# Optimization experiments

Hardware: AMD Instinct MI355X
Metric: run time of the kernel (lower is better)

The kernel has to match this reference:

```python
import jax, jax.numpy as jnp
import numpy as np

IN_CAPS = 1152
OUT_CAPS = 10
IN_DIM = 8
OUT_DIM = 16
ROUTING_ITERS = 3
BATCH = 512


def squash(s, axis=-1, eps=1e-8):
    # v = (||s||^2 / (1 + ||s||^2)) * s / ||s||
    mag_sq = jnp.sum(s * s, axis=axis, keepdims=True)
    mag = jnp.sqrt(mag_sq + eps)
    return (mag_sq / (1.0 + mag_sq)) * (s / mag)


def setup_inputs() -> dict:
    key = jax.random.key(0)
    kx, kw = jax.random.split(key)
    x = jax.random.normal(kx, (BATCH, IN_CAPS, IN_DIM), dtype=jnp.float32)
    stdv = 1.0 / np.sqrt(IN_CAPS)
    W = jax.random.uniform(kw, (IN_CAPS, OUT_CAPS, OUT_DIM, IN_DIM),
                           minval=-stdv, maxval=stdv, dtype=jnp.float32)
    return {"x": x, "W": W}


def reference(x, W):
    # u_hat[b,i,j,:] = W[i,j] @ x[b,i]  -> [B, 1152, 10, 16]
    u_hat = jnp.einsum('ijde,bie->bijd', W, x)
    u_det = jax.lax.stop_gradient(u_hat)
    b = jnp.zeros((x.shape[0], IN_CAPS, OUT_CAPS), dtype=x.dtype)
    v = None
    for it in range(ROUTING_ITERS):
        c = jax.nn.softmax(b, axis=2)  # softmax over out capsules
        u = u_hat if it == ROUTING_ITERS - 1 else u_det
        s = jnp.einsum('bij,bijd->bjd', c, u)  # [B, 10, 16]
        v = squash(s, axis=-1)
        if it != ROUTING_ITERS - 1:
            # agreement: u_hat . v  -> [B, 1152, 10]
            b = b + jnp.einsum('bijd,bjd->bij', u_det, v)
    return v  # [B, 10, 16]
```

## Files before the change

### kernel.cpp

```cpp
#include <hip/hip_runtime.h>
#include <math.h>

#define J 10
#define BT 16
#define NBT 32
#define NIC 16
#define ICB 72
#define IPW 18
#define JD 160
#define BATCH 512
#define IN_CAPS 1152
#define RTH 256

typedef __attribute__((ext_vector_type(8))) short short8;
typedef __attribute__((ext_vector_type(4))) float f32x4;
typedef __attribute__((ext_vector_type(4))) unsigned uint4v;

__device__ inline short f2bf(float f) {
    union { float f; unsigned u; } v; v.f = f;
    return (short)((v.u + 0x7FFFu + ((v.u >> 16) & 1u)) >> 16);
}
__device__ inline short8 cvt8(float4 a, float4 b) {
    short8 o;
    o[0] = f2bf(a.x); o[1] = f2bf(a.y); o[2] = f2bf(a.z); o[3] = f2bf(a.w);
    o[4] = f2bf(b.x); o[5] = f2bf(b.y); o[6] = f2bf(b.z); o[7] = f2bf(b.w);
    return o;
}
__device__ inline float bf2f(short s) {
    union { unsigned u; float f; } v; v.u = ((unsigned)(unsigned short)s) << 16;
    return v.f;
}

__global__ __launch_bounds__(256) void convert_w(
    const float* __restrict__ W, short* __restrict__ Wb, short* __restrict__ zb)
{
    const int t = blockIdx.x * 256 + threadIdx.x;
    const float4* src = (const float4*)W + (size_t)t * 2;
    *(short8*)(Wb + (size_t)t * 8) = cvt8(src[0], src[1]);
    if (blockIdx.x == 0 && threadIdx.x < 32) zb[threadIdx.x] = 0;
}

#define TI 32
#define TB 64
__global__ __launch_bounds__(256) void transpose_x(
    const float* __restrict__ X, short* __restrict__ Xb)
{
    __shared__ short8 tile[TI][TB + 1];
    const int it = blockIdx.x % (IN_CAPS / TI);
    const int bt = blockIdx.x / (IN_CAPS / TI);
    const int t  = threadIdx.x;

    const int i_l = t & 31, b_s = t >> 5;
#pragma unroll
    for (int p = 0; p < 8; ++p) {
        const int b_l = p * 8 + b_s;
        const float4* src = (const float4*)(X +
            (((size_t)(bt * TB + b_l)) * IN_CAPS + it * TI + i_l) * 8);
        tile[i_l][b_l] = cvt8(src[0], src[1]);
    }
    __syncthreads();
    const int b_l = t & 63, i_s = t >> 6;
#pragma unroll
    for (int p = 0; p < 8; ++p) {
        const int i_l2 = p * 4 + i_s;
        *(short8*)(Xb + (((size_t)(it * TI + i_l2)) * BATCH + bt * TB + b_l) * 8)
            = tile[i_l2][b_l];
    }
}

template<int MODE>
__global__ __launch_bounds__(RTH, 2) void route_kernel(
    const short* __restrict__ Xb, const short* __restrict__ Wb,
    const short* __restrict__ zb, const float* __restrict__ V,
    float* __restrict__ S_part)
{
    __shared__ float s_lds[BT][JD + 1];
    const int tid   = threadIdx.x;
    const int lane  = tid & 63, wave = tid >> 6;
    const int icb   = blockIdx.x % NIC;
    const int btile = blockIdx.x / NIC;
    const int bcol  = lane & 15, kg = lane >> 4;
    const int b     = btile * BT + bcol;

    for (int t = tid; t < BT * (JD + 1); t += RTH) (&s_lds[0][0])[t] = 0.f;
    __syncthreads();

    if (MODE == 0) {
        f32x4 acc[J];
#pragma unroll
        for (int j = 0; j < J; ++j) acc[j] = (f32x4)(0.f);
        for (int ks = wave; ks < ICB / 4; ks += 4) {
            const int ia = icb * ICB + ks * 4 + kg;
            const short8 bfr = *(const short8*)(Xb + ((size_t)ia * BATCH + b) * 8);
            short8 afr[J];
#pragma unroll
            for (int j = 0; j < J; ++j)
                afr[j] = *(const short8*)(Wb + (size_t)ia * 1280 + j * 128 + bcol * 8);
#pragma unroll
            for (int j = 0; j < J; ++j)
                acc[j] = __builtin_amdgcn_mfma_f32_16x16x32_bf16(afr[j], bfr, acc[j], 0, 0, 0);
        }
#pragma unroll
        for (int j = 0; j < J; ++j)
#pragma unroll
            for (int r = 0; r < 4; ++r)
                atomicAdd(&s_lds[bcol][j * 16 + kg * 4 + r], 0.1f * acc[j][r]);
    } else {
        float4 Vr[J];
#pragma unroll
        for (int j = 0; j < J; ++j)
            Vr[j] = *(const float4*)(V + (size_t)b * JD + j * 16 + kg * 4);

        f32x4 acc[J];
#pragma unroll
        for (int j = 0; j < J; ++j) acc[j] = (f32x4)(0.f);

        const int i0w = icb * ICB + wave * IPW;
        const short8 zero8 = (short8)(short)0;

#pragma unroll
        for (int g = 0; g < 5; ++g) {
            const int nt = (g < 4) ? 4 : 2;
            int ia = i0w + g * 4 + kg;
            if (ia > IN_CAPS - 1) ia = IN_CAPS - 1;

            short8 afr[J];
#pragma unroll
            for (int j = 0; j < J; ++j)
                afr[j] = *(const short8*)(Wb + (size_t)ia * 1280 + j * 128 + bcol * 8);
            const short8 bfull = *(const short8*)(Xb + ((size_t)ia * BATCH + b) * 8);

            float xf[8];
#pragma unroll
            for (int e = 0; e < 8; ++e) xf[e] = bf2f(bfull[e]);

            float Lp[4][J];
#pragma unroll
            for (int t = 0; t < 4; ++t) {
                if (t < nt) {
                    const short8 bt = (kg == t) ? bfull : zero8;
#pragma unroll
                    for (int j = 0; j < J; ++j) {
                        const f32x4 u = __builtin_amdgcn_mfma_f32_16x16x32_bf16(
                            afr[j], bt, (f32x4)(0.f), 0, 0, 0);
                        Lp[t][j] = u[0] * Vr[j].x + u[1] * Vr[j].y
                                 + u[2] * Vr[j].z + u[3] * Vr[j].w;
                    }
                }
            }

            float cSel[J];
#pragma unroll
            for (int j = 0; j < J; ++j) cSel[j] = 0.f;
#pragma unroll
            for (int t = 0; t < 4; ++t) {
                if (t < nt) {
                    float c[J], Z = 0.f;
#pragma unroll
                    for (int j = 0; j < J; ++j) {
                        float l = Lp[t][j];
                        l += __shfl_xor(l, 16);
                        l += __shfl_xor(l, 32);
                        c[j] = __expf(l);
                        Z += c[j];
                    }
                    const float rz = 1.0f / Z;
#pragma unroll
                    for (int j = 0; j < J; ++j) {
                        const float cv = c[j] * rz;
                        cSel[j] = (kg == t) ? cv : cSel[j];
                    }
                }
            }

#pragma unroll
            for (int j = 0; j < J; ++j) {
                const float cj = cSel[j];
                unsigned q0, q1, q2, q3;
                asm("v_cvt_pk_bf16_f32 %0, %1, %2" : "=v"(q0)
                    : "v"(xf[0] * cj), "v"(xf[1] * cj));
                asm("v_cvt_pk_bf16_f32 %0, %1, %2" : "=v"(q1)
                    : "v"(xf[2] * cj), "v"(xf[3] * cj));
                asm("v_cvt_pk_bf16_f32 %0, %1, %2" : "=v"(q2)
                    : "v"(xf[4] * cj), "v"(xf[5] * cj));
                asm("v_cvt_pk_bf16_f32 %0, %1, %2" : "=v"(q3)
                    : "v"(xf[6] * cj), "v"(xf[7] * cj));
                union { uint4v v; short8 s; } bu;
                bu.v = (uint4v){q0, q1, q2, q3};
                acc[j] = __builtin_amdgcn_mfma_f32_16x16x32_bf16(
                    afr[j], bu.s, acc[j], 0, 0, 0);
            }
        }
#pragma unroll
        for (int j = 0; j < J; ++j)
#pragma unroll
            for (int r = 0; r < 4; ++r)
                atomicAdd(&s_lds[bcol][j * 16 + kg * 4 + r], acc[j][r]);
    }
    __syncthreads();

    for (int t = tid; t < BT * JD; t += RTH) {
        const int bb = t / JD, p = t % JD;
        S_part[((size_t)icb * BATCH + btile * BT + bb) * JD + p] = s_lds[bb][p];
    }
}

__global__ __launch_bounds__(256) void squash_kernel(
    const float* __restrict__ S_part, float* __restrict__ V,
    float* __restrict__ out, int mode)
{
    const int t = blockIdx.x * 256 + threadIdx.x;
    float s = 0.f;
#pragma unroll
    for (int ic = 0; ic < NIC; ic++)
        s += S_part[(size_t)ic * BATCH * JD + t];
    float sq = s * s;
    sq += __shfl_xor(sq, 1);
    sq += __shfl_xor(sq, 2);
    sq += __shfl_xor(sq, 4);
    sq += __shfl_xor(sq, 8);
    const float v = s * sq / ((1.f + sq) * sqrtf(sq + 1e-8f));
    if (mode == 0)      V[t] = v;
    else if (mode == 1) V[t] += v;
    else                out[t] = v;
}

extern "C" void kernel_launch(void* const* d_in, const int* in_sizes, int n_in,
                              void* d_out, int out_size, void* d_ws, size_t ws_size,
                              hipStream_t stream)
{
    const float* X = (const float*)d_in[0];
    const float* W = (const float*)d_in[1];
    float* out = (float*)d_out;

    float* S_part = (float*)d_ws;
    float* V      = S_part + (size_t)NIC * BATCH * JD;
    short* Wb     = (short*)(V + (size_t)BATCH * JD);
    short* Xb     = Wb + (size_t)IN_CAPS * JD * 8;
    short* zb     = Xb + (size_t)IN_CAPS * BATCH * 8;

    const dim3 rg(NBT * NIC), rb(RTH);
    const dim3 sg(BATCH * JD / 256), sb(256);

    convert_w<<<dim3(720), dim3(256), 0, stream>>>(W, Wb, zb);
    transpose_x<<<dim3((IN_CAPS / TI) * (BATCH / TB)), dim3(256), 0, stream>>>(X, Xb);

    route_kernel<0><<<rg, rb, 0, stream>>>(Xb, Wb, zb, V, S_part);
    squash_kernel<<<sg, sb, 0, stream>>>(S_part, V, out, 0);
    route_kernel<1><<<rg, rb, 0, stream>>>(Xb, Wb, zb, V, S_part);
    squash_kernel<<<sg, sb, 0, stream>>>(S_part, V, out, 1);
    route_kernel<1><<<rg, rb, 0, stream>>>(Xb, Wb, zb, V, S_part);
    squash_kernel<<<sg, sb, 0, stream>>>(S_part, V, out, 2);
}
```

Measured before the change: 156.6 us.

## Reduce routing logits across lanes with f16 MFMA instead of shuffles

The agreement logits, previously reduced with cross-lane shuffles and recomputed softmax for each of four capsule slots, are now packed into fp16 B-fragments. Constant 0/1 selector matrices in fp16 MFMAs then sum them, so each lane gets its own capsule's logits directly and runs one softmax instead of four. V is prescaled by log2(e) so exp2 and a hardware reciprocal can replace expf and division. This removes shuffle and redundant exp work but adds extra MFMAs and fp16 round-toward-zero precision loss on the logit terms.

Measured after the change: 148.1 us. 5.4% less time.

```diff
diff --git a/kernel.cpp b/kernel.cpp
--- a/kernel.cpp
+++ b/kernel.cpp
@@ -11,10 +11,12 @@
 #define BATCH 512
 #define IN_CAPS 1152
 #define RTH 256
+#define LOG2E 1.4426950408889634f
 
 typedef __attribute__((ext_vector_type(8))) short short8;
 typedef __attribute__((ext_vector_type(4))) float f32x4;
-typedef __attribute__((ext_vector_type(4))) unsigned uint4v;
+typedef __attribute__((ext_vector_type(8))) __fp16 fp16x8;
+typedef __attribute__((ext_vector_type(2))) __fp16 fp16x2;
 
 __device__ inline short f2bf(float f) {
     union { float f; unsigned u; } v; v.f = f;
@@ -108,12 +110,24 @@
     } else {
         float4 Vr[J];
 #pragma unroll
-        for (int j = 0; j < J; ++j)
-            Vr[j] = *(const float4*)(V + (size_t)b * JD + j * 16 + kg * 4);
+        for (int j = 0; j < J; ++j) {
+            float4 v4 = *(const float4*)(V + (size_t)b * JD + j * 16 + kg * 4);
+            v4.x *= LOG2E; v4.y *= LOG2E; v4.z *= LOG2E; v4.w *= LOG2E;
+            Vr[j] = v4;
+        }
 
         f32x4 acc[J];
 #pragma unroll
         for (int j = 0; j < J; ++j) acc[j] = (f32x4)(0.f);
+
+        fp16x8 a1f, a2f;
+#pragma unroll
+        for (int e = 0; e < 8; ++e) {
+            const bool in1 = (bcol < 4) ? (e < 4) : ((bcol < 8) ? (e >= 4) : false);
+            const bool in2 = (bcol >= 12) ? (e >= 4) : ((bcol >= 8) ? (e < 4) : false);
+            a1f[e] = in1 ? (__fp16)1.0f : (__fp16)0.0f;
+            a2f[e] = in2 ? (__fp16)1.0f : (__fp16)0.0f;
+        }
 
         const int i0w = icb * ICB + wave * IPW;
         const short8 zero8 = (short8)(short)0;
@@ -134,48 +148,57 @@
 #pragma unroll
             for (int e = 0; e < 8; ++e) xf[e] = bf2f(bfull[e]);
 
-            float Lp[4][J];
+            fp16x8 B1[J], B2[J];
 #pragma unroll
             for (int t = 0; t < 4; ++t) {
                 if (t < nt) {
-                    const short8 bt = (kg == t) ? bfull : zero8;
+                    const short8 btf = (kg == t) ? bfull : zero8;
 #pragma unroll
                     for (int j = 0; j < J; ++j) {
                         const f32x4 u = __builtin_amdgcn_mfma_f32_16x16x32_bf16(
-                            afr[j], bt, (f32x4)(0.f), 0, 0, 0);
-                        Lp[t][j] = u[0] * Vr[j].x + u[1] * Vr[j].y
-                                 + u[2] * Vr[j].z + u[3] * Vr[j].w;
+                            afr[j], btf, (f32x4)(0.f), 0, 0, 0);
+                        const fp16x2 pa = __builtin_amdgcn_cvt_pkrtz(
+                            u[0] * Vr[j].x, u[1] * Vr[j].y);
+                        const fp16x2 pc = __builtin_amdgcn_cvt_pkrtz(
+                            u[2] * Vr[j].z, u[3] * Vr[j].w);
+                        fp16x8& Bt = (t < 2) ? B1[j] : B2[j];
+                        const int o = (t & 1) * 4;
+                        Bt[o + 0] = pa[0]; Bt[o + 1] = pa[1];
+                        Bt[o + 2] = pc[0]; Bt[o + 3] = pc[1];
                     }
                 }
             }
 
-            float cSel[J];
-#pragma unroll
-            for (int j = 0; j < J; ++j) cSel[j] = 0.f;
-#pragma unroll
-            for (int t = 0; t < 4; ++t) {
-                if (t < nt) {
-                    float c[J], Z = 0.f;
-#pragma unroll
-                    for (int j = 0; j < J; ++j) {
-                        float l = Lp[t][j];
-                        l += __shfl_xor(l, 16);
-                        l += __shfl_xor(l, 32);
-                        c[j] = __expf(l);
-                        Z += c[j];
-                    }
-                    const float rz = 1.0f / Z;
-#pragma unroll
-                    for (int j = 0; j < J; ++j) {
-                        const float cv = c[j] * rz;
-                        cSel[j] = (kg == t) ? cv : cSel[j];
-                    }
+            float L[J];
+            if (nt == 4) {
+#pragma unroll
+                for (int j = 0; j < J; ++j) {
+                    const f32x4 l1 = __builtin_amdgcn_mfma_f32_16x16x32_f16(
+                        a1f, B1[j], (f32x4)(0.f), 0, 0, 0);
+                    const f32x4 l2 = __builtin_amdgcn_mfma_f32_16x16x32_f16(
+                        a2f, B2[j], (f32x4)(0.f), 0, 0, 0);
+                    L[j] = l1[0] + l2[0];
+                }
+            } else {
+#pragma unroll
+                for (int j = 0; j < J; ++j) {
+                    const f32x4 l1 = __builtin_amdgcn_mfma_f32_16x16x32_f16(
+                        a1f, B1[j], (f32x4)(0.f), 0, 0, 0);
+                    L[j] = l1[0];
                 }
             }
 
+            float c[J];
+#pragma unroll
+            for (int j = 0; j < J; ++j) c[j] = __builtin_exp2f(L[j]);
+            const float Z = ((c[0] + c[1]) + (c[2] + c[3]))
+                          + (((c[4] + c[5]) + (c[6] + c[7])) + (c[8] + c[9]));
+            const float rz = __builtin_amdgcn_rcpf(Z);
+
 #pragma unroll
             for (int j = 0; j < J; ++j) {
-                const float cj = cSel[j];
+                float cj = c[j] * rz;
+                if (nt != 4) cj = (kg < 2) ? cj : 0.f;
                 unsigned q0, q1, q2, q3;
                 asm("v_cvt_pk_bf16_f32 %0, %1, %2" : "=v"(q0)
                     : "v"(xf[0] * cj), "v"(xf[1] * cj));
@@ -185,8 +208,8 @@
                     : "v"(xf[4] * cj), "v"(xf[5] * cj));
                 asm("v_cvt_pk_bf16_f32 %0, %1, %2" : "=v"(q3)
                     : "v"(xf[6] * cj), "v"(xf[7] * cj));
-                union { uint4v v; short8 s; } bu;
-                bu.v = (uint4v){q0, q1, q2, q3};
+                union { unsigned u[4]; short8 s; } bu;
+                bu.u[0] = q0; bu.u[1] = q1; bu.u[2] = q2; bu.u[3] = q3;
                 acc[j] = __builtin_amdgcn_mfma_f32_16x16x32_bf16(
                     afr[j], bu.s, acc[j], 0, 0, 0);
             }
```
